# Kernel tuning notes

Hardware: AMD Instinct MI355X
Metric: run time of the kernel (lower is better)

The kernel has to match this reference:

```python
import jax, jax.numpy as jnp
import numpy as np

B, TX, DH, U2 = 32, 2048, 512, 1024  # batch, src len, decoder dim, 2*units

def setup_inputs() -> dict:
    key = jax.random.key(0)
    ks = jax.random.split(key, 8)
    a = jax.random.normal(ks[0], (B, TX, U2), jnp.float32)
    h = jax.random.normal(ks[1], (B, DH), jnp.float32)
    coverage = jax.random.uniform(ks[2], (B, TX), jnp.float32)
    X_mask = jax.random.randint(ks[3], (B, TX, 1), 0, 2).astype(bool)
    s = 1.0 / np.sqrt(U2)
    Wa = jax.random.normal(ks[4], (U2, U2), jnp.float32) * s
    Wh_w = jax.random.normal(ks[5], (DH, U2), jnp.float32) / np.sqrt(DH)
    Wh_b = jnp.zeros((U2,), jnp.float32)
    Wc = jax.random.normal(ks[6], (1, U2), jnp.float32)
    v = jax.random.normal(ks[7], (U2, 1), jnp.float32) * s
    return {"a": a, "h": h, "coverage": coverage, "X_mask": X_mask,
            "Wa": Wa, "Wh_w": Wh_w, "Wh_b": Wh_b, "Wc": Wc, "v": v,
            "use_coverage": 1, "use_masking": 1}

def reference(a, h, coverage, X_mask, Wa, Wh_w, Wh_b, Wc, v,
              use_coverage, use_masking):
    # encoder features: [B,Tx,2u]
    enc = jnp.einsum('btd,de->bte', a, Wa)
    # decoder features broadcast over Tx (RepeatVector): [B,1,2u]
    dec = (h @ Wh_w + Wh_b)[:, None, :]
    feats = enc + dec
    if use_coverage:
        # coverage [B,Tx] -> [B,Tx,1] @ Wc[1,2u] == outer broadcast
        feats = feats + coverage[:, :, None] * Wc[0]
    e = jnp.tanh(feats) @ v                      # [B,Tx,1]
    alpha = jax.nn.softmax(e, axis=1)            # softmax over Tx
    if use_masking:
        alpha = jnp.where(X_mask, alpha, 0.0)
        alpha_sum = jnp.sum(alpha, axis=1)       # [B,1]
        alpha = jnp.squeeze(alpha, -1) / alpha_sum  # [B,Tx]
        alpha = alpha[:, :, None]
    context = jnp.sum(alpha * a, axis=1)[:, None, :]  # [B,1,2u]
    return context, jnp.squeeze(alpha, -1)
```

## Files before the change

### kernel.cpp

```cpp
#include <hip/hip_runtime.h>
#include <hip/hip_bf16.h>

#define BB  32
#define TXX 2048
#define DHH 512
#define UU  1024
#define MM  (BB*TXX)

typedef __attribute__((ext_vector_type(8))) short s8v;
typedef __attribute__((ext_vector_type(4))) float f4v;

#define GLDS16(g, l)                                                        \
  __builtin_amdgcn_global_load_lds(                                         \
      (const __attribute__((address_space(1))) void*)(g),                   \
      (__attribute__((address_space(3))) void*)(l), 16, 0, 0)

__device__ __forceinline__ ushort f2bf(float f) {
  return __builtin_bit_cast(ushort, __float2bfloat16(f));
}
__device__ __forceinline__ float bf2f(ushort u) {
  unsigned x = ((unsigned)u) << 16;
  return __builtin_bit_cast(float, x);
}

__device__ __forceinline__ float tanh_fast(float x) {
  float ax = fabsf(x);
  float e2 = __expf(-2.0f * ax);
  float t = (1.0f - e2) * __builtin_amdgcn_rcpf(1.0f + e2);
  return copysignf(t, x);
}

__device__ __forceinline__ int ldsu(int frag, int kh, int i15) {
  return (frag << 6) | (kh << 4) | (i15 ^ (kh << 2));
}

__global__ __launch_bounds__(256) void watrans_kernel(
    const float* __restrict__ Wa, ushort* __restrict__ WaT) {
  __shared__ float Ts[64][65];
  const int jb = blockIdx.x & 15, kb = blockIdx.x >> 4;
  const int c = threadIdx.x & 63, r0 = threadIdx.x >> 6;
#pragma unroll
  for (int i = 0; i < 16; ++i) {
    int kl = r0 + 4 * i;
    Ts[c][kl] = Wa[(size_t)(kb * 64 + kl) * UU + jb * 64 + c];
  }
  __syncthreads();
#pragma unroll
  for (int i = 0; i < 16; ++i) {
    int jl = r0 + 4 * i;
    WaT[(size_t)(jb * 64 + jl) * UU + kb * 64 + c] = f2bf(Ts[jl][c]);
  }
}

__global__ __launch_bounds__(256) void a2bf_kernel(
    const float* __restrict__ a, ushort* __restrict__ abf) {
  const size_t i = ((size_t)blockIdx.x * 256 + threadIdx.x) * 8;
  float4 v0 = *(const float4*)(a + i);
  float4 v1 = *(const float4*)(a + i + 4);
  ushort u[8] = {f2bf(v0.x), f2bf(v0.y), f2bf(v0.z), f2bf(v0.w),
                 f2bf(v1.x), f2bf(v1.y), f2bf(v1.z), f2bf(v1.w)};
  *(uint4*)(abf + i) = *(const uint4*)u;
}

__global__ __launch_bounds__(256) void dec_kernel(
    const float* __restrict__ h, const float* __restrict__ Whw,
    const float* __restrict__ Whb, float* __restrict__ dec) {
  const int b = blockIdx.x >> 2, c = blockIdx.x & 3;
  __shared__ float hs[DHH];
  for (int k = threadIdx.x; k < DHH; k += 256) hs[k] = h[b * DHH + k];
  __syncthreads();
  const int j = c * 256 + threadIdx.x;
  float acc = Whb[j];
#pragma unroll 8
  for (int k = 0; k < DHH; ++k) acc = fmaf(hs[k], Whw[(size_t)k * UU + j], acc);
  dec[b * UU + j] = acc;
}

__global__ __launch_bounds__(512, 1) void e_mfma8_kernel(
    const ushort* __restrict__ abf, const ushort* __restrict__ WaT,
    const float* __restrict__ dec, const float* __restrict__ cov,
    const float* __restrict__ Wc, const float* __restrict__ v,
    const int* __restrict__ use_cov_p, float* __restrict__ partial) {
  __shared__ __align__(16) ushort aS[32768];
  __shared__ __align__(16) ushort bS[32768];
  __shared__ float dec_s[256], v_s[256], wc_s[256], cov_s[256];
  __shared__ float peL[4][256];

  const int tid = threadIdx.x;
  const int lane = tid & 63;
  const int w = tid >> 6;
  const int wm = w >> 2, wn = w & 3;

  const int x = blockIdx.x & 7;
  const int r = blockIdx.x >> 3;
  const int nt = r & 3;
  const int mt = (r >> 2) * 8 + x;

  const int j0 = nt * 256;
  const int row0 = mt * 256;
  const int b = row0 >> 11;
  const int trow0 = row0 & (TXX - 1);

  if (tid < 256) {
    dec_s[tid] = dec[b * UU + j0 + tid];
    v_s[tid] = v[j0 + tid];
    wc_s[tid] = Wc[j0 + tid];
    cov_s[tid] = (*use_cov_p) ? cov[b * TXX + trow0 + tid] : 0.0f;
  }

  f4v acc[8][4];
#pragma unroll
  for (int mi = 0; mi < 8; ++mi)
#pragma unroll
    for (int ni = 0; ni < 4; ++ni) acc[mi][ni] = (f4v){0.f, 0.f, 0.f, 0.f};

  const ushort* __restrict__ aT = abf + (size_t)row0 * UU;
  const ushort* __restrict__ bT = WaT + (size_t)j0 * UU;
  const int i15 = lane & 15, khl = lane >> 4;

  auto stageA = [&](int kt, int ns, int kf) {
#pragma unroll
    for (int l = 0; l < 2; ++l) {
      const int frag = l * 8 + w;
      GLDS16(aT + (size_t)(frag * 16 + i15) * UU + kt * 64 + kf * 32 + khl * 8,
             &aS[ns * 16384 + kf * 8192 + (l * 512 + w * 64) * 8]);
    }
  };
  auto stageB = [&](int kt, int ns, int kf) {
#pragma unroll
    for (int l = 0; l < 2; ++l) {
      const int frag = l * 8 + w;
      GLDS16(bT + (size_t)(frag * 16 + i15) * UU + kt * 64 + kf * 32 + khl * 8,
             &bS[ns * 16384 + kf * 8192 + (l * 512 + w * 64) * 8]);
    }
  };
  auto readA = [&](s8v af[4], int slot, int kf, int mh) {
#pragma unroll
    for (int q = 0; q < 4; ++q) {
      const int frag = wm * 8 + mh * 4 + q;
      af[q] = *(const s8v*)&aS[slot * 16384 + kf * 8192 + frag * 512 + lane * 8];
    }
  };
  auto readB = [&](s8v bf[4], int slot, int kf) {
#pragma unroll
    for (int q = 0; q < 4; ++q) {
      const int frag = wn * 4 + q;
      bf[q] = *(const s8v*)&bS[slot * 16384 + kf * 8192 + frag * 512 + lane * 8];
    }
  };

#define MFMA16(MH)                                                          \
  do {                                                                      \
    __builtin_amdgcn_s_setprio(1);                                          \
    _Pragma("unroll")                                                       \
    for (int q = 0; q < 4; ++q)                                             \
      _Pragma("unroll")                                                     \
      for (int ni = 0; ni < 4; ++ni)                                        \
        acc[(MH)*4 + q][ni] = __builtin_amdgcn_mfma_f32_16x16x32_bf16(      \
            af[q], bf[ni], acc[(MH)*4 + q][ni], 0, 0, 0);                   \
    __builtin_amdgcn_s_setprio(0);                                          \
  } while (0)

#define VMBAR(N)                                                            \
  asm volatile("s_waitcnt vmcnt(" #N ")" ::: "memory");                     \
  __builtin_amdgcn_s_barrier();                                             \
  __builtin_amdgcn_sched_barrier(0)

  stageA(0, 0, 0); stageB(0, 0, 0); stageA(0, 0, 1); stageB(0, 0, 1);

  for (int t = 0; t < 16; ++t) {
    const int slot = t & 1, ns = slot ^ 1;
    s8v af[4], bf[4];
    if (t < 15) { stageA(t + 1, ns, 0); VMBAR(6); } else { VMBAR(4); }
    readB(bf, slot, 0);
    readA(af, slot, 0, 0);
    MFMA16(0);
    if (t < 15) stageB(t + 1, ns, 0);
    readA(af, slot, 0, 1);
    MFMA16(1);
    if (t < 15) { stageA(t + 1, ns, 1); VMBAR(6); } else { VMBAR(0); }
    readB(bf, slot, 1);
    readA(af, slot, 1, 0);
    MFMA16(0);
    if (t < 15) stageB(t + 1, ns, 1);
    readA(af, slot, 1, 1);
    MFMA16(1);
  }
#undef VMBAR
#undef MFMA16

  const int lj = lane & 15, lk = lane >> 4;
#pragma unroll
  for (int mi = 0; mi < 8; ++mi) {
#pragma unroll
    for (int r2 = 0; r2 < 4; ++r2) {
      const int rowl = wm * 128 + mi * 16 + lk * 4 + r2;
      const float cv = cov_s[rowl];
      float s = 0.f;
#pragma unroll
      for (int ni = 0; ni < 4; ++ni) {
        const int jl = wn * 64 + ni * 16 + lj;
        float f = acc[mi][ni][r2] + dec_s[jl] + cv * wc_s[jl];
        s += v_s[jl] * tanh_fast(f);
      }
      s += __shfl_xor(s, 1); s += __shfl_xor(s, 2);
      s += __shfl_xor(s, 4); s += __shfl_xor(s, 8);
      if (lj == 0) peL[wn][rowl] = s;
    }
  }
  __syncthreads();
  if (tid < 256)
    partial[(size_t)nt * MM + row0 + tid] =
        peL[0][tid] + peL[1][tid] + peL[2][tid] + peL[3][tid];
}

__device__ __forceinline__ void e_epilogue8(
    f4v acc[4][4], const float* dec_s, const float* v_s, const float* wc_s,
    const float* cov_s, float peL[2][128], int lane, int wm, int wn,
    float* __restrict__ partial, int nt, int row0, int tid) {
  const int lj = lane & 15, lk = lane >> 4;
#pragma unroll
  for (int mi = 0; mi < 4; ++mi) {
#pragma unroll
    for (int r = 0; r < 4; ++r) {
      const int rowl = (wm << 6) + (mi << 4) + (lk << 2) + r;
      const float cv = cov_s[rowl];
      float s = 0.f;
#pragma unroll
      for (int ni = 0; ni < 4; ++ni) {
        const int jl = (wn << 6) + (ni << 4) + lj;
        float f = acc[mi][ni][r] + dec_s[jl] + cv * wc_s[jl];
        s += v_s[jl] * tanh_fast(f);
      }
      s += __shfl_xor(s, 1); s += __shfl_xor(s, 2);
      s += __shfl_xor(s, 4); s += __shfl_xor(s, 8);
      if (lj == 0) peL[wn][rowl] = s;
    }
  }
  __syncthreads();
  if (tid < 128)
    partial[(size_t)nt * MM + row0 + tid] = peL[0][tid] + peL[1][tid];
}

__global__ __launch_bounds__(256) void e_mfma_slow_kernel(
    const float* __restrict__ a, const ushort* __restrict__ WaT,
    const float* __restrict__ dec, const float* __restrict__ cov,
    const float* __restrict__ Wc, const float* __restrict__ v,
    const int* __restrict__ use_cov_p, float* __restrict__ partial) {
  __shared__ __align__(16) ushort aS[4096];
  __shared__ __align__(16) ushort bS[4096];
  __shared__ float dec_s[128], v_s[128], wc_s[128], cov_s[128];
  __shared__ float peL[2][128];

  const int tid = threadIdx.x;
  const int lane = tid & 63;
  const int wid = tid >> 6;
  const int wm = wid >> 1, wn = wid & 1;

  const int x = blockIdx.x & 7;
  const int q = blockIdx.x >> 3;
  const int nt = q & 7;
  const int mt = (q >> 3) * 8 + x;

  const int j0 = nt * 128;
  const int row0 = mt * 128;
  const int b = row0 >> 11;
  const int trow0 = row0 & (TXX - 1);

  if (tid < 128) {
    dec_s[tid] = dec[b * UU + j0 + tid];
    v_s[tid] = v[j0 + tid];
    wc_s[tid] = Wc[j0 + tid];
    cov_s[tid] = (*use_cov_p) ? cov[b * TXX + trow0 + tid] : 0.0f;
  }

  f4v zero = {0.f, 0.f, 0.f, 0.f};
  f4v acc[4][4];
#pragma unroll
  for (int mi = 0; mi < 4; ++mi)
#pragma unroll
    for (int ni = 0; ni < 4; ++ni) acc[mi][ni] = zero;

  const float* __restrict__ aRow = a + (size_t)row0 * UU;
  const int arow = tid >> 3;
  const int kq = (tid & 7) * 4;
  const int jrow = tid >> 2;
  const int kc = tid & 3;

  for (int ks = 0; ks < 32; ++ks) {
    const int k0 = ks * 32;
#pragma unroll
    for (int l = 0; l < 4; ++l) {
      const int row = l * 32 + arow;
      float4 va = *(const float4*)(aRow + (size_t)row * UU + k0 + kq);
      ushort4 ub = make_ushort4(f2bf(va.x), f2bf(va.y), f2bf(va.z), f2bf(va.w));
      const int unit = ldsu(row >> 4, kq >> 3, row & 15);
      *(ushort4*)&aS[unit * 8 + (kq & 7)] = ub;
    }
#pragma unroll
    for (int l = 0; l < 2; ++l) {
      const int jr = l * 64 + jrow;
      uint4 wv = *(const uint4*)(WaT + (size_t)(j0 + jr) * UU + k0 + kc * 8);
      *(uint4*)&bS[ldsu(jr >> 4, kc, jr & 15) * 8] = wv;
    }
    __syncthreads();
    s8v af[4], bff[4];
    const int kh = lane >> 4, i15 = lane & 15;
#pragma unroll
    for (int mi = 0; mi < 4; ++mi)
      af[mi] = *(const s8v*)&aS[ldsu((wm << 2) + mi, kh, i15) * 8];
#pragma unroll
    for (int ni = 0; ni < 4; ++ni)
      bff[ni] = *(const s8v*)&bS[ldsu((wn << 2) + ni, kh, i15) * 8];
#pragma unroll
    for (int mi = 0; mi < 4; ++mi)
#pragma unroll
      for (int ni = 0; ni < 4; ++ni)
        acc[mi][ni] = __builtin_amdgcn_mfma_f32_16x16x32_bf16(af[mi], bff[ni], acc[mi][ni], 0, 0, 0);
    __syncthreads();
  }

  e_epilogue8(acc, dec_s, v_s, wc_s, cov_s, peL, lane, wm, wn, partial, nt, row0, tid);
}

__global__ __launch_bounds__(256) void softmax_kernel(
    const float* __restrict__ partial, const void* __restrict__ mask,
    const int* __restrict__ use_mask_p, float* __restrict__ alpha, int npart) {
  int b = blockIdx.x;
  int tid = threadIdx.x;
  int lane = tid & 63, wv = tid >> 6;
  const unsigned char* m8 = (const unsigned char*)mask;
  const int* m32 = (const int*)mask;
  int um = *use_mask_p;

  __shared__ int isBoolS;
  if (tid == 0) isBoolS = 0;

  __shared__ float es[TXX];
  for (int t = tid; t < TXX; t += 256) {
    float s = 0.f;
    for (int nt = 0; nt < npart; ++nt) s += partial[(size_t)nt * MM + b * TXX + t];
    es[t] = s;
  }
  __syncthreads();
  {
    uint4 qq = ((const uint4*)mask)[tid];
    unsigned nz = (qq.x | qq.y | qq.z | qq.w) & 0xFFFFFF00u;
    if (nz) atomicOr(&isBoolS, 1);
  }
  __syncthreads();
  const int isBool = isBoolS;

  float m = -1e30f;
  for (int t = tid; t < TXX; t += 256) m = fmaxf(m, es[t]);
#pragma unroll
  for (int o = 32; o > 0; o >>= 1) m = fmaxf(m, __shfl_xor(m, o, 64));
  __shared__ float redm[4];
  if (lane == 0) redm[wv] = m;
  __syncthreads();
  m = fmaxf(fmaxf(redm[0], redm[1]), fmaxf(redm[2], redm[3]));

  float s = 0.f;
  for (int t = tid; t < TXX; t += 256) {
    float w = __expf(es[t] - m);
    if (um) {
      int mv = isBool ? (int)m8[b * TXX + t] : m32[b * TXX + t];
      if (mv == 0) w = 0.f;
    }
    s += w;
  }
#pragma unroll
  for (int o = 32; o > 0; o >>= 1) s += __shfl_xor(s, o, 64);
  __shared__ float reds[4];
  if (lane == 0) reds[wv] = s;
  __syncthreads();
  s = reds[0] + reds[1] + reds[2] + reds[3];
  float inv = 1.0f / s;

  for (int t = tid; t < TXX; t += 256) {
    float w = __expf(es[t] - m);
    if (um) {
      int mv = isBool ? (int)m8[b * TXX + t] : m32[b * TXX + t];
      if (mv == 0) w = 0.f;
    }
    alpha[b * TXX + t] = w * inv;
  }
}

__global__ __launch_bounds__(256) void context_bf_kernel(
    const ushort* __restrict__ abf, const float* __restrict__ alpha,
    float* __restrict__ cpart) {
  const int b = blockIdx.x >> 4;
  const int ts = blockIdx.x & 15;
  const int th = threadIdx.x >> 7;
  const int c = threadIdx.x & 127;
  const int dc = c * 8;
  const ushort* __restrict__ ab = abf + (size_t)(b * TXX + ts * 128) * UU + dc;
  const float* __restrict__ alb = alpha + b * TXX + ts * 128;
  float acc[8] = {0.f, 0.f, 0.f, 0.f, 0.f, 0.f, 0.f, 0.f};
  for (int t = th; t < 128; t += 2) {
    float al = alb[t];
    union { uint4 q; ushort us[8]; } Q;
    Q.q = *(const uint4*)(ab + (size_t)t * UU);
#pragma unroll
    for (int u = 0; u < 8; ++u) acc[u] = fmaf(al, bf2f(Q.us[u]), acc[u]);
  }
  __shared__ float s2[2][128][8];
#pragma unroll
  for (int u = 0; u < 8; ++u) s2[th][c][u] = acc[u];
  __syncthreads();
  if (th == 0) {
    float o[8];
#pragma unroll
    for (int u = 0; u < 8; ++u) o[u] = s2[0][c][u] + s2[1][c][u];
    float* dst = cpart + (size_t)(ts * BB + b) * UU + dc;
    *(float4*)dst = make_float4(o[0], o[1], o[2], o[3]);
    *(float4*)(dst + 4) = make_float4(o[4], o[5], o[6], o[7]);
  }
}

__global__ __launch_bounds__(256) void context_f32_kernel(
    const float* __restrict__ a, const float* __restrict__ alpha,
    float* __restrict__ cpart) {
  const int b = blockIdx.x >> 4;
  const int ts = blockIdx.x & 15;
  const int d4 = threadIdx.x * 4;
  const float* __restrict__ ab  = a + (size_t)(b * TXX + ts * 128) * UU;
  const float* __restrict__ alb = alpha + b * TXX + ts * 128;
  float4 acc = {0.f, 0.f, 0.f, 0.f};
  for (int t = 0; t < 128; t += 4) {
#pragma unroll
    for (int u = 0; u < 4; ++u) {
      float al = alb[t + u];
      float4 va = *(const float4*)(ab + (size_t)(t + u) * UU + d4);
      acc.x = fmaf(al, va.x, acc.x);
      acc.y = fmaf(al, va.y, acc.y);
      acc.z = fmaf(al, va.z, acc.z);
      acc.w = fmaf(al, va.w, acc.w);
    }
  }
  *(float4*)(cpart + (size_t)(ts * BB + b) * UU + d4) = acc;
}

__global__ __launch_bounds__(256) void ctx_reduce_kernel(
    const float* __restrict__ cpart, float* __restrict__ ctx) {
  int i = blockIdx.x * 256 + threadIdx.x;
  float s = 0.f;
#pragma unroll
  for (int ts = 0; ts < 16; ++ts) s += cpart[(size_t)ts * BB * UU + i];
  ctx[i] = s;
}

extern "C" void kernel_launch(void* const* d_in, const int* in_sizes, int n_in,
                              void* d_out, int out_size, void* d_ws, size_t ws_size,
                              hipStream_t stream) {
  const float* a   = (const float*)d_in[0];
  const float* h   = (const float*)d_in[1];
  const float* cov = (const float*)d_in[2];
  const void*  msk = d_in[3];
  const float* Wa  = (const float*)d_in[4];
  const float* Whw = (const float*)d_in[5];
  const float* Whb = (const float*)d_in[6];
  const float* Wc  = (const float*)d_in[7];
  const float* v   = (const float*)d_in[8];
  const int* use_cov  = (const int*)d_in[9];
  const int* use_mask = (const int*)d_in[10];

  float*  dec     = (float*)d_ws;
  ushort* WaT     = (ushort*)((char*)d_ws + 131072);
  float*  partial = (float*)((char*)d_ws + 131072 + 2097152);
  float*  cpart   = partial;
  ushort* abf     = (ushort*)((char*)d_ws + 4325376);
  const size_t need = 4325376 + (size_t)MM * UU * 2;

  float* ctx   = (float*)d_out;
  float* alpha = (float*)d_out + BB * UU;

  watrans_kernel<<<256, 256, 0, stream>>>(Wa, WaT);
  dec_kernel<<<BB * 4, 256, 0, stream>>>(h, Whw, Whb, dec);
  if (ws_size >= need) {
    a2bf_kernel<<<(int)((size_t)MM * UU / 8 / 256), 256, 0, stream>>>(a, abf);
    e_mfma8_kernel<<<(MM / 256) * 4, 512, 0, stream>>>(abf, WaT, dec, cov, Wc, v, use_cov, partial);
    softmax_kernel<<<BB, 256, 0, stream>>>(partial, msk, use_mask, alpha, 4);
    context_bf_kernel<<<BB * 16, 256, 0, stream>>>(abf, alpha, cpart);
  } else {
    e_mfma_slow_kernel<<<(MM / 128) * 8, 256, 0, stream>>>(a, WaT, dec, cov, Wc, v, use_cov, partial);
    softmax_kernel<<<BB, 256, 0, stream>>>(partial, msk, use_mask, alpha, 8);
    context_f32_kernel<<<BB * 16, 256, 0, stream>>>(a, alpha, cpart);
  }
  ctx_reduce_kernel<<<BB * UU / 256, 256, 0, stream>>>(cpart, ctx);
}
```

Before: 321.2 us.

## Restructure GEMM main loop into ping-pong barrier schedule with peeled epilogue

Reorders the bf16 MFMA main loop so that LDS fragment reads and the global-to-LDS staging of the next tile are issued before a barrier, and each MFMA block is bracketed by barriers with an lgkmcnt wait. The vmcnt waits become separate and the last iteration is peeled out of the loop. The aim is to let waves alternate between memory issue and MFMA phases, hiding load latency better. The cost is more barriers per iteration, which could add synchronization stalls.

```diff
diff --git a/kernel.cpp b/kernel.cpp
--- a/kernel.cpp
+++ b/kernel.cpp
@@ -161,32 +161,58 @@
     __builtin_amdgcn_s_setprio(0);                                          \
   } while (0)
 
-#define VMBAR(N)                                                            \
-  asm volatile("s_waitcnt vmcnt(" #N ")" ::: "memory");                     \
+#define BAR_LGKM                                                            \
   __builtin_amdgcn_s_barrier();                                             \
+  asm volatile("s_waitcnt lgkmcnt(0)" ::: "memory");                        \
   __builtin_amdgcn_sched_barrier(0)
 
+#define CLOSE_BAR __builtin_amdgcn_s_barrier()
+
+#define VM(N) asm volatile("s_waitcnt vmcnt(" #N ")" ::: "memory")
+
   stageA(0, 0, 0); stageB(0, 0, 0); stageA(0, 0, 1); stageB(0, 0, 1);
-
-  for (int t = 0; t < 16; ++t) {
+  VM(4);
+  __builtin_amdgcn_s_barrier();
+  __builtin_amdgcn_sched_barrier(0);
+
+  s8v af[4], bf[4];
+  for (int t = 0; t < 15; ++t) {
     const int slot = t & 1, ns = slot ^ 1;
-    s8v af[4], bf[4];
-    if (t < 15) { stageA(t + 1, ns, 0); VMBAR(6); } else { VMBAR(4); }
-    readB(bf, slot, 0);
-    readA(af, slot, 0, 0);
+    readB(bf, slot, 0); readA(af, slot, 0, 0);
+    stageA(t + 1, ns, 0);
+    BAR_LGKM;
     MFMA16(0);
-    if (t < 15) stageB(t + 1, ns, 0);
+    CLOSE_BAR;
     readA(af, slot, 0, 1);
+    stageB(t + 1, ns, 0);
+    VM(4);
+    BAR_LGKM;
     MFMA16(1);
-    if (t < 15) { stageA(t + 1, ns, 1); VMBAR(6); } else { VMBAR(0); }
-    readB(bf, slot, 1);
-    readA(af, slot, 1, 0);
+    CLOSE_BAR;
+    readB(bf, slot, 1); readA(af, slot, 1, 0);
+    stageA(t + 1, ns, 1);
+    BAR_LGKM;
     MFMA16(0);
-    if (t < 15) stageB(t + 1, ns, 1);
+    CLOSE_BAR;
     readA(af, slot, 1, 1);
+    stageB(t + 1, ns, 1);
+    VM(4);
+    BAR_LGKM;
     MFMA16(1);
-  }
-#undef VMBAR
+    CLOSE_BAR;
+  }
+  readB(bf, 1, 0); readA(af, 1, 0, 0);
+  BAR_LGKM; MFMA16(0); CLOSE_BAR;
+  readA(af, 1, 0, 1);
+  VM(0);
+  BAR_LGKM; MFMA16(1); CLOSE_BAR;
+  readB(bf, 1, 1); readA(af, 1, 1, 0);
+  BAR_LGKM; MFMA16(0); CLOSE_BAR;
+  readA(af, 1, 1, 1);
+  BAR_LGKM; MFMA16(1);
+#undef VM
+#undef CLOSE_BAR
+#undef BAR_LGKM
 #undef MFMA16
 
   const int lj = lane & 15, lk = lane >> 4;
```

After: 367.0 us. 1.14x slower.

## Replace 512-thread 256x256 GEMM tile with two-block-per-CU 256x128 tiles

Applied to the files above, without the earlier changes.

The encoder-score GEMM kernel moves from one 512-thread block per CU computing a 256x256 tile to 256-thread blocks computing a 256x128 tile, with two blocks allowed per CU. The K loop becomes a simpler 32-step double-buffered pipeline using one combined A+B stage and a full vmcnt(0) barrier each step. Output is split into 8 column partials instead of 4, and the softmax reduction count changes to match. The aim is to overlap work across two resident blocks instead of relying on fine-grained intra-block scheduling. In exchange, A is re-read twice as often and the per-iteration full wait may expose load latency.

```diff
diff --git a/kernel.cpp b/kernel.cpp
--- a/kernel.cpp
+++ b/kernel.cpp
@@ -76,37 +76,37 @@
   dec[b * UU + j] = acc;
 }
 
-__global__ __launch_bounds__(512, 1) void e_mfma8_kernel(
+__global__ __launch_bounds__(256, 2) void e_mfma2b_kernel(
     const ushort* __restrict__ abf, const ushort* __restrict__ WaT,
     const float* __restrict__ dec, const float* __restrict__ cov,
     const float* __restrict__ Wc, const float* __restrict__ v,
     const int* __restrict__ use_cov_p, float* __restrict__ partial) {
-  __shared__ __align__(16) ushort aS[32768];
-  __shared__ __align__(16) ushort bS[32768];
-  __shared__ float dec_s[256], v_s[256], wc_s[256], cov_s[256];
-  __shared__ float peL[4][256];
+  __shared__ __align__(16) ushort aS[16384];
+  __shared__ __align__(16) ushort bS[8192];
+  __shared__ float dec_s[128], v_s[128], wc_s[128], cov_s[256];
+  __shared__ float peL[2][256];
 
   const int tid = threadIdx.x;
   const int lane = tid & 63;
   const int w = tid >> 6;
-  const int wm = w >> 2, wn = w & 3;
+  const int wm = w >> 1, wn = w & 1;
 
   const int x = blockIdx.x & 7;
-  const int r = blockIdx.x >> 3;
-  const int nt = r & 3;
-  const int mt = (r >> 2) * 8 + x;
-
-  const int j0 = nt * 256;
+  const int q = blockIdx.x >> 3;
+  const int nt = q & 7;
+  const int mt = (q >> 3) * 8 + x;
+
+  const int j0 = nt * 128;
   const int row0 = mt * 256;
   const int b = row0 >> 11;
   const int trow0 = row0 & (TXX - 1);
 
-  if (tid < 256) {
+  if (tid < 128) {
     dec_s[tid] = dec[b * UU + j0 + tid];
     v_s[tid] = v[j0 + tid];
     wc_s[tid] = Wc[j0 + tid];
-    cov_s[tid] = (*use_cov_p) ? cov[b * TXX + trow0 + tid] : 0.0f;
-  }
+  }
+  cov_s[tid] = (*use_cov_p) ? cov[b * TXX + trow0 + tid] : 0.0f;
 
   f4v acc[8][4];
 #pragma unroll
@@ -118,76 +118,49 @@
   const ushort* __restrict__ bT = WaT + (size_t)j0 * UU;
   const int i15 = lane & 15, khl = lane >> 4;
 
-  auto stageA = [&](int kt, int ns, int kf) {
+  auto stage = [&](int kt, int ns) {
+    const int k0 = kt * 32 + khl * 8;
+#pragma unroll
+    for (int l = 0; l < 4; ++l) {
+      const int f = l * 4 + w;
+      GLDS16(aT + (size_t)(f * 16 + i15) * UU + k0, &aS[ns * 8192 + f * 512]);
+    }
 #pragma unroll
     for (int l = 0; l < 2; ++l) {
-      const int frag = l * 8 + w;
-      GLDS16(aT + (size_t)(frag * 16 + i15) * UU + kt * 64 + kf * 32 + khl * 8,
-             &aS[ns * 16384 + kf * 8192 + (l * 512 + w * 64) * 8]);
+      const int f = l * 4 + w;
+      GLDS16(bT + (size_t)(f * 16 + i15) * UU + k0, &bS[ns * 4096 + f * 512]);
     }
   };
-  auto stageB = [&](int kt, int ns, int kf) {
-#pragma unroll
-    for (int l = 0; l < 2; ++l) {
-      const int frag = l * 8 + w;
-      GLDS16(bT + (size_t)(frag * 16 + i15) * UU + kt * 64 + kf * 32 + khl * 8,
-             &bS[ns * 16384 + kf * 8192 + (l * 512 + w * 64) * 8]);
-    }
-  };
-  auto readA = [&](s8v af[4], int slot, int kf, int mh) {
-#pragma unroll
-    for (int q = 0; q < 4; ++q) {
-      const int frag = wm * 8 + mh * 4 + q;
-      af[q] = *(const s8v*)&aS[slot * 16384 + kf * 8192 + frag * 512 + lane * 8];
-    }
-  };
-  auto readB = [&](s8v bf[4], int slot, int kf) {
-#pragma unroll
-    for (int q = 0; q < 4; ++q) {
-      const int frag = wn * 4 + q;
-      bf[q] = *(const s8v*)&bS[slot * 16384 + kf * 8192 + frag * 512 + lane * 8];
-    }
-  };
-
-#define MFMA16(MH)                                                          \
-  do {                                                                      \
-    __builtin_amdgcn_s_setprio(1);                                          \
-    _Pragma("unroll")                                                       \
-    for (int q = 0; q < 4; ++q)                                             \
-      _Pragma("unroll")                                                     \
-      for (int ni = 0; ni < 4; ++ni)                                        \
-        acc[(MH)*4 + q][ni] = __builtin_amdgcn_mfma_f32_16x16x32_bf16(      \
-            af[q], bf[ni], acc[(MH)*4 + q][ni], 0, 0, 0);                   \
-    __builtin_amdgcn_s_setprio(0);                                          \
-  } while (0)
-
-#define VMBAR(N)                                                            \
-  asm volatile("s_waitcnt vmcnt(" #N ")" ::: "memory");                     \
+
+#define VMBAR0                                                              \
+  asm volatile("s_waitcnt vmcnt(0)" ::: "memory");                          \
   __builtin_amdgcn_s_barrier();                                             \
   __builtin_amdgcn_sched_barrier(0)
 
-  stageA(0, 0, 0); stageB(0, 0, 0); stageA(0, 0, 1); stageB(0, 0, 1);
-
-  for (int t = 0; t < 16; ++t) {
+  stage(0, 0);
+  VMBAR0;
+
+  for (int t = 0; t < 32; ++t) {
     const int slot = t & 1, ns = slot ^ 1;
-    s8v af[4], bf[4];
-    if (t < 15) { stageA(t + 1, ns, 0); VMBAR(6); } else { VMBAR(4); }
-    readB(bf, slot, 0);
-    readA(af, slot, 0, 0);
-    MFMA16(0);
-    if (t < 15) stageB(t + 1, ns, 0);
-    readA(af, slot, 0, 1);
-    MFMA16(1);
-    if (t < 15) { stageA(t + 1, ns, 1); VMBAR(6); } else { VMBAR(0); }
-    readB(bf, slot, 1);
-    readA(af, slot, 1, 0);
-    MFMA16(0);
-    if (t < 15) stageB(t + 1, ns, 1);
-    readA(af, slot, 1, 1);
-    MFMA16(1);
-  }
-#undef VMBAR
-#undef MFMA16
+    if (t < 31) stage(t + 1, ns);
+    s8v af[8], bf[4];
+#pragma unroll
+    for (int ni = 0; ni < 4; ++ni)
+      bf[ni] = *(const s8v*)&bS[slot * 4096 + (wn * 4 + ni) * 512 + lane * 8];
+#pragma unroll
+    for (int mi = 0; mi < 8; ++mi)
+      af[mi] = *(const s8v*)&aS[slot * 8192 + (wm * 8 + mi) * 512 + lane * 8];
+    __builtin_amdgcn_s_setprio(1);
+#pragma unroll
+    for (int mi = 0; mi < 8; ++mi)
+#pragma unroll
+      for (int ni = 0; ni < 4; ++ni)
+        acc[mi][ni] = __builtin_amdgcn_mfma_f32_16x16x32_bf16(
+            af[mi], bf[ni], acc[mi][ni], 0, 0, 0);
+    __builtin_amdgcn_s_setprio(0);
+    if (t < 31) { VMBAR0; }
+  }
+#undef VMBAR0
 
   const int lj = lane & 15, lk = lane >> 4;
 #pragma unroll
@@ -209,9 +182,7 @@
     }
   }
   __syncthreads();
-  if (tid < 256)
-    partial[(size_t)nt * MM + row0 + tid] =
-        peL[0][tid] + peL[1][tid] + peL[2][tid] + peL[3][tid];
+  partial[(size_t)nt * MM + row0 + tid] = peL[0][tid] + peL[1][tid];
 }
 
 __device__ __forceinline__ void e_epilogue8(
@@ -480,8 +451,8 @@
   dec_kernel<<<BB * 4, 256, 0, stream>>>(h, Whw, Whb, dec);
   if (ws_size >= need) {
     a2bf_kernel<<<(int)((size_t)MM * UU / 8 / 256), 256, 0, stream>>>(a, abf);
-    e_mfma8_kernel<<<(MM / 256) * 4, 512, 0, stream>>>(abf, WaT, dec, cov, Wc, v, use_cov, partial);
-    softmax_kernel<<<BB, 256, 0, stream>>>(partial, msk, use_mask, alpha, 4);
+    e_mfma2b_kernel<<<(MM / 256) * 8, 256, 0, stream>>>(abf, WaT, dec, cov, Wc, v, use_cov, partial);
+    softmax_kernel<<<BB, 256, 0, stream>>>(partial, msk, use_mask, alpha, 8);
     context_bf_kernel<<<BB * 16, 256, 0, stream>>>(abf, alpha, cpart);
   } else {
     e_mfma_slow_kernel<<<(MM / 128) * 8, 256, 0, stream>>>(a, WaT, dec, cov, Wc, v, use_cov, partial);
```

After: 375.9 us. 17.0% more time.
